# Kernel tuning notes

Measured on AMD Instinct MI355X. Metric: run time of the kernel, lower is better.

The kernel has to match this reference:

```python
import jax, jax.numpy as jnp
import numpy as np

N_NODES = 100000


def gcn_conv(x, W, b, src, dst, n_nodes):
    # PyG GCNConv: h = x @ W; add self-loops; sym-normalized scatter-add; + bias
    loop = jnp.arange(n_nodes, dtype=src.dtype)
    src2 = jnp.concatenate([src, loop])
    dst2 = jnp.concatenate([dst, loop])
    deg = jax.ops.segment_sum(jnp.ones(src2.shape, x.dtype), dst2, num_segments=n_nodes)
    dinv = jax.lax.rsqrt(deg)  # deg >= 1 thanks to self-loops
    norm = dinv[src2] * dinv[dst2]                 # [E+N]
    h = x @ W                                      # [N, out]
    msg = h[src2] * norm[:, None]                  # gather + scale, [E+N, out]
    out = jax.ops.segment_sum(msg, dst2, num_segments=n_nodes)  # scatter-add
    return out + b


def setup_inputs() -> dict:
    key = jax.random.key(0)
    k1, k2, k3, k4, k5 = jax.random.split(key, 5)
    nfeat, nhid = 128, 64
    n_edges = 1600000
    x = jax.random.normal(k1, (N_NODES, nfeat), dtype=jnp.float32)
    edge_index = jax.random.randint(k2, (2, n_edges), 0, N_NODES, dtype=jnp.int64)
    W1 = jax.random.normal(k3, (nfeat, nhid), dtype=jnp.float32) / np.sqrt(nfeat)
    b1 = jnp.zeros((nhid,), jnp.float32)
    W2 = jax.random.normal(k4, (nhid, nhid), dtype=jnp.float32) / np.sqrt(nhid)
    b2 = jnp.zeros((nhid,), jnp.float32)
    return {"x": x, "edge_index": edge_index, "W1": W1, "b1": b1, "W2": W2, "b2": b2}


def reference(x, edge_index, W1, b1, W2, b2):
    # eval mode: dropout is identity
    src, dst = edge_index[0], edge_index[1]
    h = jax.nn.relu(gcn_conv(x, W1, b1, src, dst, N_NODES))
    residual = h
    out = jax.nn.relu(gcn_conv(h, W2, b2, src, dst, N_NODES))
    return out + residual
```

## Files before the change

### kernel.cpp

```cpp
#include <hip/hip_runtime.h>

#define N_NODES 100000
#define NDUMMY 100000
#define NH 64
#define NB 500
#define NPB 200
#define BCAP 4096
#define PBCAP 6400
#define EPB 8192


__device__ __forceinline__ unsigned short f2bf(float f) {
    union { float f; unsigned int i; } c;
    c.f = f;
    unsigned int b = c.i;
    b += 0x7FFFu + ((b >> 16) & 1u);
    return (unsigned short)(b >> 16);
}

__device__ __forceinline__ unsigned pack2bf(float lo, float hi) {
    return (unsigned)f2bf(lo) | ((unsigned)f2bf(hi) << 16);
}

__device__ __forceinline__ float bfLO(unsigned u) {
    union { unsigned i; float f; } c; c.i = u << 16; return c.f;
}
__device__ __forceinline__ float bfHI(unsigned u) {
    union { unsigned i; float f; } c; c.i = u & 0xFFFF0000u; return c.f;
}


__global__ __launch_bounds__(512) void k_init(int* __restrict__ bcur, unsigned* __restrict__ dummy_row) {
    int t = threadIdx.x;
    if (t < NB) bcur[t] = 0;
    if (t < 32) dummy_row[t] = 0;
}


__global__ __launch_bounds__(1024) void k_sort(const int* __restrict__ src, const int* __restrict__ dst,
                                               int* __restrict__ bcur, unsigned* __restrict__ ebuf, int e) {
    __shared__ unsigned sorted[EPB];
    __shared__ unsigned short cellof[EPB];
    __shared__ int lh[512];
    __shared__ int lbase[512];
    __shared__ int lcur[512];
    __shared__ int gpos[512];
    __shared__ int wsum[8];
    const int t = threadIdx.x;
    const int e0 = blockIdx.x * EPB;
    int cnt = e - e0; if (cnt > EPB) cnt = EPB;

    if (t < 512) lh[t] = 0;
    __syncthreads();

    for (int i = t * 4; i < cnt; i += 4096) {
        int4 d4 = *(const int4*)&dst[e0 + i];
        atomicAdd(&lh[d4.x / NPB], 1);
        atomicAdd(&lh[d4.y / NPB], 1);
        atomicAdd(&lh[d4.z / NPB], 1);
        atomicAdd(&lh[d4.w / NPB], 1);
    }
    __syncthreads();

    const int lane = t & 63, wave = t >> 6;
    int v = 0, inc = 0;
    if (t < 512) {
        v = (t < NB) ? lh[t] : 0;
        inc = v;
#pragma unroll
        for (int d = 1; d < 64; d <<= 1) {
            int u = __shfl_up(inc, d, 64);
            if (lane >= d) inc += u;
        }
        if (lane == 63) wsum[wave] = inc;
    }
    __syncthreads();
    if (t < NB) {
        int woff = 0;
#pragma unroll
        for (int w = 0; w < 8; ++w)
            if (w < wave) woff += wsum[w];
        const int excl = woff + inc - v;
        lbase[t] = excl;
        lcur[t] = excl;
        gpos[t] = atomicAdd(&bcur[t], v);
    }
    __syncthreads();

    for (int i = t * 4; i < cnt; i += 4096) {
        int4 d4 = *(const int4*)&dst[e0 + i];
        int4 s4 = *(const int4*)&src[e0 + i];
        int b0 = d4.x / NPB, b1 = d4.y / NPB, b2 = d4.z / NPB, b3 = d4.w / NPB;
        int p0 = atomicAdd(&lcur[b0], 1);
        int p1 = atomicAdd(&lcur[b1], 1);
        int p2 = atomicAdd(&lcur[b2], 1);
        int p3 = atomicAdd(&lcur[b3], 1);
        sorted[p0] = ((unsigned)(d4.x - b0 * NPB) << 17) | (unsigned)s4.x; cellof[p0] = (unsigned short)b0;
        sorted[p1] = ((unsigned)(d4.y - b1 * NPB) << 17) | (unsigned)s4.y; cellof[p1] = (unsigned short)b1;
        sorted[p2] = ((unsigned)(d4.z - b2 * NPB) << 17) | (unsigned)s4.z; cellof[p2] = (unsigned short)b2;
        sorted[p3] = ((unsigned)(d4.w - b3 * NPB) << 17) | (unsigned)s4.w; cellof[p3] = (unsigned short)b3;
    }
    __syncthreads();

    for (int i = t * 4; i < cnt; i += 4096) {
        uint4 sv = *(const uint4*)&sorted[i];
        ushort4 cv = *(const ushort4*)&cellof[i];
        int c0 = cv.x, c1 = cv.y, c2 = cv.z, c3 = cv.w;
        int g0 = gpos[c0] + (i + 0 - lbase[c0]);
        int g1 = gpos[c1] + (i + 1 - lbase[c1]);
        int g2 = gpos[c2] + (i + 2 - lbase[c2]);
        int g3 = gpos[c3] + (i + 3 - lbase[c3]);
        if (g0 < BCAP) ebuf[(long long)c0 * BCAP + g0] = sv.x;
        if (g1 < BCAP) ebuf[(long long)c1 * BCAP + g1] = sv.y;
        if (g2 < BCAP) ebuf[(long long)c2 * BCAP + g2] = sv.z;
        if (g3 < BCAP) ebuf[(long long)c3 * BCAP + g3] = sv.w;
    }
}

__global__ __launch_bounds__(256) void k_build(const unsigned* __restrict__ ebuf, const int* __restrict__ bcur,
                                               int* __restrict__ rowptr, int* __restrict__ degp,
                                               float* __restrict__ dinv, int* __restrict__ csrc, int n) {
    __shared__ unsigned ls[BCAP];
    __shared__ int lh[256];
    __shared__ int lpv[256];
    __shared__ int lstart[256];
    __shared__ int lc[256];
    __shared__ int wsum[4];
    const int b = blockIdx.x;
    const int t = threadIdx.x;
    const int node0 = b * NPB;
    int count = bcur[b];
    if (count > BCAP) count = BCAP;
    const int rbase = b * PBCAP;

    lh[t] = 0;
    for (int i = t; i < count; i += 256) ls[i] = ebuf[(long long)b * BCAP + i];
    __syncthreads();
    for (int i = t; i < count; i += 256) atomicAdd(&lh[ls[i] >> 17], 1);
    __syncthreads();

    const int v = lh[t];
    lpv[t] = (v + 7) & ~7;
    __syncthreads();
    const int g = t & ~7;
    int pvg = lpv[g];
#pragma unroll
    for (int j = 1; j < 8; ++j) pvg = max(pvg, lpv[g + j]);

    const int lane = t & 63, wave = t >> 6;
    int inc = pvg;
#pragma unroll
    for (int d = 1; d < 64; d <<= 1) {
        int u = __shfl_up(inc, d, 64);
        if (lane >= d) inc += u;
    }
    if (lane == 63) wsum[wave] = inc;
    __syncthreads();
    int woff = 0;
#pragma unroll
    for (int w = 0; w < 4; ++w)
        if (w < wave) woff += wsum[w];
    const int start = rbase + woff + inc - pvg;

    lstart[t] = start;
    lc[t] = start;
    const int node = node0 + t;
    if (t < NPB && node < n) {
        rowptr[node] = start;
        degp[node] = pvg;
        dinv[node] = rsqrtf((float)(v + 1));
    }
    __syncthreads();

    for (int i = t; i < count; i += 256) {
        unsigned u = ls[i];
        int pos = atomicAdd(&lc[u >> 17], 1);
        csrc[pos] = (int)(u & 0x1FFFFu);
    }
    __syncthreads();

    const int pend = lstart[t] + pvg;
    for (int p = lc[t]; p < pend; ++p) csrc[p] = NDUMMY;
}


typedef __attribute__((ext_vector_type(8))) short bf16x8;
typedef __attribute__((ext_vector_type(4))) float f32x4;

template <int K>
__global__ __launch_bounds__(256) void k_gemm_mfma(const float* __restrict__ X, const float* __restrict__ W,
                                                   const float* __restrict__ dinv,
                                                   unsigned short* __restrict__ out, int n) {
    constexpr int KH = K / 2;
    constexpr int WP = (K == 128) ? 68 : 40;
    constexpr int NKS = K / 32;
    __shared__ unsigned wsb[64][WP];
    const int tid = threadIdx.x;
    const int lane = tid & 63;
    const int wv = tid >> 6;
    const int n0 = blockIdx.x * 64;
    const int col = lane & 15;
    const int q = lane >> 4;

    const int row = n0 + wv * 16 + col;
    const int rc = (row < n) ? row : (n - 1);
    const float* xp = X + (long long)rc * K + q * 8;
    float4 xa[NKS], xb[NKS];
#pragma unroll
    for (int ks = 0; ks < NKS; ++ks) {
        xa[ks] = *(const float4*)&xp[ks * 32];
        xb[ks] = *(const float4*)&xp[ks * 32 + 4];
    }

    for (int idx = tid; idx < 64 * KH; idx += 256) {
        int c = idx & 63, k2 = idx >> 6;
        wsb[c][k2] = pack2bf(W[(2 * k2) * NH + c], W[(2 * k2 + 1) * NH + c]);
    }

    union FragU { bf16x8 v; unsigned u[4]; };
    bf16x8 afrag[NKS];
#pragma unroll
    for (int ks = 0; ks < NKS; ++ks) {
        FragU f;
        f.u[0] = pack2bf(xa[ks].x, xa[ks].y);
        f.u[1] = pack2bf(xa[ks].z, xa[ks].w);
        f.u[2] = pack2bf(xb[ks].x, xb[ks].y);
        f.u[3] = pack2bf(xb[ks].z, xb[ks].w);
        afrag[ks] = f.v;
    }
    __syncthreads();

    f32x4 zero = {0.f, 0.f, 0.f, 0.f};
    f32x4 acc[4];
#pragma unroll
    for (int nt = 0; nt < 4; ++nt) acc[nt] = zero;

#pragma unroll
    for (int ks = 0; ks < NKS; ++ks) {
#pragma unroll
        for (int nt = 0; nt < 4; ++nt) {
            bf16x8 b = *(const bf16x8*)&wsb[nt * 16 + col][ks * 16 + q * 4];
            acc[nt] = __builtin_amdgcn_mfma_f32_16x16x32_bf16(afrag[ks], b, acc[nt], 0, 0, 0);
        }
    }

#pragma unroll
    for (int r = 0; r < 4; ++r) {
        int node = n0 + wv * 16 + q * 4 + r;
        if (node < n) {
            float dv = dinv[node];
#pragma unroll
            for (int nt = 0; nt < 4; ++nt)
                out[(long long)node * NH + nt * 16 + col] = f2bf(acc[nt][r] * dv);
        }
    }
}


__global__ __launch_bounds__(256) void k_agg(const unsigned* __restrict__ hs32, const float* __restrict__ dinv,
                                             const int* __restrict__ rowptr, const int* __restrict__ degp,
                                             const int* __restrict__ csrc,
                                             const float* __restrict__ bias, const float* __restrict__ resid,
                                             float* __restrict__ out, int n) {
    const int gt = blockIdx.x * 256 + threadIdx.x;
    const int wave = gt >> 6;
    const int lane = threadIdx.x & 63;
    const int sub = lane >> 3;
    const int li = lane & 7;
    const int node = wave * 8 + sub;
    if (node >= n) return;

    const uint4* hsv = (const uint4*)hs32;
    uint4 su = hsv[node * 8 + li];
    float a0 = bfLO(su.x), a1 = bfHI(su.x), a2 = bfLO(su.y), a3 = bfHI(su.y);
    float a4 = bfLO(su.z), a5 = bfHI(su.z), a6 = bfLO(su.w), a7 = bfHI(su.w);
    float b0 = 0.f, b1 = 0.f, b2 = 0.f, b3 = 0.f, b4 = 0.f, b5 = 0.f, b6 = 0.f, b7 = 0.f;

    const int rp = rowptr[node];
    const int dg = degp[node];
    int4 c0, c1;
    if (dg > 0) {
        c0 = *(const int4*)&csrc[rp];
        c1 = *(const int4*)&csrc[rp + 4];
    }
    for (int e = 0; e < dg; e += 8) {
        const int4 m0 = c0, m1 = c1;
        if (e + 8 < dg) {
            c0 = *(const int4*)&csrc[rp + e + 8];
            c1 = *(const int4*)&csrc[rp + e + 12];
        }
        uint4 u0 = hsv[m0.x * 8 + li];
        uint4 u1 = hsv[m0.y * 8 + li];
        uint4 u2 = hsv[m0.z * 8 + li];
        uint4 u3 = hsv[m0.w * 8 + li];
        uint4 u4 = hsv[m1.x * 8 + li];
        uint4 u5 = hsv[m1.y * 8 + li];
        uint4 u6 = hsv[m1.z * 8 + li];
        uint4 u7 = hsv[m1.w * 8 + li];
        a0 += bfLO(u0.x); a1 += bfHI(u0.x); a2 += bfLO(u0.y); a3 += bfHI(u0.y);
        a4 += bfLO(u0.z); a5 += bfHI(u0.z); a6 += bfLO(u0.w); a7 += bfHI(u0.w);
        b0 += bfLO(u1.x); b1 += bfHI(u1.x); b2 += bfLO(u1.y); b3 += bfHI(u1.y);
        b4 += bfLO(u1.z); b5 += bfHI(u1.z); b6 += bfLO(u1.w); b7 += bfHI(u1.w);
        a0 += bfLO(u2.x); a1 += bfHI(u2.x); a2 += bfLO(u2.y); a3 += bfHI(u2.y);
        a4 += bfLO(u2.z); a5 += bfHI(u2.z); a6 += bfLO(u2.w); a7 += bfHI(u2.w);
        b0 += bfLO(u3.x); b1 += bfHI(u3.x); b2 += bfLO(u3.y); b3 += bfHI(u3.y);
        b4 += bfLO(u3.z); b5 += bfHI(u3.z); b6 += bfLO(u3.w); b7 += bfHI(u3.w);
        a0 += bfLO(u4.x); a1 += bfHI(u4.x); a2 += bfLO(u4.y); a3 += bfHI(u4.y);
        a4 += bfLO(u4.z); a5 += bfHI(u4.z); a6 += bfLO(u4.w); a7 += bfHI(u4.w);
        b0 += bfLO(u5.x); b1 += bfHI(u5.x); b2 += bfLO(u5.y); b3 += bfHI(u5.y);
        b4 += bfLO(u5.z); b5 += bfHI(u5.z); b6 += bfLO(u5.w); b7 += bfHI(u5.w);
        a0 += bfLO(u6.x); a1 += bfHI(u6.x); a2 += bfLO(u6.y); a3 += bfHI(u6.y);
        a4 += bfLO(u6.z); a5 += bfHI(u6.z); a6 += bfLO(u6.w); a7 += bfHI(u6.w);
        b0 += bfLO(u7.x); b1 += bfHI(u7.x); b2 += bfLO(u7.y); b3 += bfHI(u7.y);
        b4 += bfLO(u7.z); b5 += bfHI(u7.z); b6 += bfLO(u7.w); b7 += bfHI(u7.w);
    }
    const float dv = dinv[node];
    const float4 ba = *(const float4*)&bias[8 * li];
    const float4 bb = *(const float4*)&bias[8 * li + 4];
    float v0 = fmaxf(dv * (a0 + b0) + ba.x, 0.f);
    float v1 = fmaxf(dv * (a1 + b1) + ba.y, 0.f);
    float v2 = fmaxf(dv * (a2 + b2) + ba.z, 0.f);
    float v3 = fmaxf(dv * (a3 + b3) + ba.w, 0.f);
    float v4 = fmaxf(dv * (a4 + b4) + bb.x, 0.f);
    float v5 = fmaxf(dv * (a5 + b5) + bb.y, 0.f);
    float v6 = fmaxf(dv * (a6 + b6) + bb.z, 0.f);
    float v7 = fmaxf(dv * (a7 + b7) + bb.w, 0.f);
    const long long ob = (long long)node * NH + 8 * li;
    if (resid) {
        float4 r0 = *(const float4*)&resid[ob];
        float4 r1 = *(const float4*)&resid[ob + 4];
        v0 += r0.x; v1 += r0.y; v2 += r0.z; v3 += r0.w;
        v4 += r1.x; v5 += r1.y; v6 += r1.z; v7 += r1.w;
    }
    *(float4*)&out[ob] = make_float4(v0, v1, v2, v3);
    *(float4*)&out[ob + 4] = make_float4(v4, v5, v6, v7);
}


extern "C" void kernel_launch(void* const* d_in, const int* in_sizes, int n_in,
                              void* d_out, int out_size, void* d_ws, size_t ws_size,
                              hipStream_t stream) {
    const float* x  = (const float*)d_in[0];
    const int*   ei = (const int*)d_in[1];
    const float* W1 = (const float*)d_in[2];
    const float* b1 = (const float*)d_in[3];
    const float* W2 = (const float*)d_in[4];
    const float* b2 = (const float*)d_in[5];
    float* out = (float*)d_out;

    const int N = N_NODES;
    const int E = in_sizes[1] / 2;
    const int* src = ei;
    const int* dst = ei + E;

    const int NP = 100352;
    int*   bcur   = (int*)d_ws;
    int*   rowptr = bcur + 512;
    int*   degp   = rowptr + NP;
    float* dinv   = (float*)(degp + NP);
    int*   csrc   = (int*)(dinv + NP);
    unsigned* ebuf = (unsigned*)(csrc + NB * PBCAP);
    unsigned* hs32 = ebuf;
    unsigned short* hsb = (unsigned short*)hs32;
    float* h1     = (float*)(hs32 + (long long)(NDUMMY + 1) * 32);

    const int nb_sort = (E + EPB - 1) / EPB;

    k_init<<<1, 512, 0, stream>>>(bcur, hs32 + (long long)NDUMMY * 32);
    k_sort<<<nb_sort, 1024, 0, stream>>>(src, dst, bcur, ebuf, E);
    k_build<<<NB, 256, 0, stream>>>(ebuf, bcur, rowptr, degp, dinv, csrc, N);

    k_gemm_mfma<128><<<(N + 63) / 64, 256, 0, stream>>>(x, W1, dinv, hsb, N);
    k_agg<<<(N + 31) / 32, 256, 0, stream>>>(hs32, dinv, rowptr, degp, csrc, b1, nullptr, h1, N);

    k_gemm_mfma<64><<<(N + 63) / 64, 256, 0, stream>>>(h1, W2, dinv, hsb, N);
    k_agg<<<(N + 31) / 32, 256, 0, stream>>>(hs32, dinv, rowptr, degp, csrc, b2, h1, out, N);
}
```

Before: 131.3 us.

## Split bf16 feature table into two 32-column halves for cache-friendlier aggregation

The GEMM now writes the bf16 hidden features as two separate planes, each holding 32 columns per node, and the aggregation kernel launches twice as many blocks, each block handling one half. Each gathered plane is half the size of the full table, so it is more likely to stay resident in L2/MALL while the random neighbour gathers run. In exchange, every neighbour index is read twice, per-lane loads shrink from 16 to 8 bytes, and the workspace is reordered so the sort buffer aliases h1.

```diff
diff --git a/kernel.cpp b/kernel.cpp
--- a/kernel.cpp
+++ b/kernel.cpp
@@ -2,6 +2,7 @@
 
 #define N_NODES 100000
 #define NDUMMY 100000
+#define NROWS 100001
 #define NH 64
 #define NB 500
 #define NPB 200
@@ -30,10 +31,14 @@
 }
 
 
-__global__ __launch_bounds__(512) void k_init(int* __restrict__ bcur, unsigned* __restrict__ dummy_row) {
+__global__ __launch_bounds__(512) void k_init(int* __restrict__ bcur, unsigned* __restrict__ hs32) {
     int t = threadIdx.x;
     if (t < NB) bcur[t] = 0;
-    if (t < 32) dummy_row[t] = 0;
+    if (t >= 512 - 32) {
+        int j = t - (512 - 32);
+        int h = j >> 4, w = j & 15;
+        hs32[(long long)h * NROWS * 16 + (long long)NDUMMY * 16 + w] = 0;
+    }
 }
 
 
@@ -250,8 +255,11 @@
         if (node < n) {
             float dv = dinv[node];
 #pragma unroll
-            for (int nt = 0; nt < 4; ++nt)
-                out[(long long)node * NH + nt * 16 + col] = f2bf(acc[nt][r] * dv);
+            for (int nt = 0; nt < 4; ++nt) {
+                int c = nt * 16 + col;
+                long long addr = (long long)(c >> 5) * NROWS * 32 + (long long)node * 32 + (c & 31);
+                out[addr] = f2bf(acc[nt][r] * dv);
+            }
         }
     }
 }
@@ -262,19 +270,19 @@
                                              const int* __restrict__ csrc,
                                              const float* __restrict__ bias, const float* __restrict__ resid,
                                              float* __restrict__ out, int n) {
-    const int gt = blockIdx.x * 256 + threadIdx.x;
-    const int wave = gt >> 6;
+    const int h = blockIdx.x & 1;
+    const int nb = blockIdx.x >> 1;
+    const int wave_in_blk = threadIdx.x >> 6;
     const int lane = threadIdx.x & 63;
     const int sub = lane >> 3;
     const int li = lane & 7;
-    const int node = wave * 8 + sub;
+    const int node = nb * 32 + wave_in_blk * 8 + sub;
     if (node >= n) return;
 
-    const uint4* hsv = (const uint4*)hs32;
-    uint4 su = hsv[node * 8 + li];
+    const uint2* hsv = (const uint2*)(hs32 + (long long)h * NROWS * 16);
+    uint2 su = hsv[node * 8 + li];
     float a0 = bfLO(su.x), a1 = bfHI(su.x), a2 = bfLO(su.y), a3 = bfHI(su.y);
-    float a4 = bfLO(su.z), a5 = bfHI(su.z), a6 = bfLO(su.w), a7 = bfHI(su.w);
-    float b0 = 0.f, b1 = 0.f, b2 = 0.f, b3 = 0.f, b4 = 0.f, b5 = 0.f, b6 = 0.f, b7 = 0.f;
+    float b0 = 0.f, b1 = 0.f, b2 = 0.f, b3 = 0.f;
 
     const int rp = rowptr[node];
     const int dg = degp[node];
@@ -289,51 +297,36 @@
             c0 = *(const int4*)&csrc[rp + e + 8];
             c1 = *(const int4*)&csrc[rp + e + 12];
         }
-        uint4 u0 = hsv[m0.x * 8 + li];
-        uint4 u1 = hsv[m0.y * 8 + li];
-        uint4 u2 = hsv[m0.z * 8 + li];
-        uint4 u3 = hsv[m0.w * 8 + li];
-        uint4 u4 = hsv[m1.x * 8 + li];
-        uint4 u5 = hsv[m1.y * 8 + li];
-        uint4 u6 = hsv[m1.z * 8 + li];
-        uint4 u7 = hsv[m1.w * 8 + li];
+        uint2 u0 = hsv[m0.x * 8 + li];
+        uint2 u1 = hsv[m0.y * 8 + li];
+        uint2 u2 = hsv[m0.z * 8 + li];
+        uint2 u3 = hsv[m0.w * 8 + li];
+        uint2 u4 = hsv[m1.x * 8 + li];
+        uint2 u5 = hsv[m1.y * 8 + li];
+        uint2 u6 = hsv[m1.z * 8 + li];
+        uint2 u7 = hsv[m1.w * 8 + li];
         a0 += bfLO(u0.x); a1 += bfHI(u0.x); a2 += bfLO(u0.y); a3 += bfHI(u0.y);
-        a4 += bfLO(u0.z); a5 += bfHI(u0.z); a6 += bfLO(u0.w); a7 += bfHI(u0.w);
         b0 += bfLO(u1.x); b1 += bfHI(u1.x); b2 += bfLO(u1.y); b3 += bfHI(u1.y);
-        b4 += bfLO(u1.z); b5 += bfHI(u1.z); b6 += bfLO(u1.w); b7 += bfHI(u1.w);
         a0 += bfLO(u2.x); a1 += bfHI(u2.x); a2 += bfLO(u2.y); a3 += bfHI(u2.y);
-        a4 += bfLO(u2.z); a5 += bfHI(u2.z); a6 += bfLO(u2.w); a7 += bfHI(u2.w);
         b0 += bfLO(u3.x); b1 += bfHI(u3.x); b2 += bfLO(u3.y); b3 += bfHI(u3.y);
-        b4 += bfLO(u3.z); b5 += bfHI(u3.z); b6 += bfLO(u3.w); b7 += bfHI(u3.w);
         a0 += bfLO(u4.x); a1 += bfHI(u4.x); a2 += bfLO(u4.y); a3 += bfHI(u4.y);
-        a4 += bfLO(u4.z); a5 += bfHI(u4.z); a6 += bfLO(u4.w); a7 += bfHI(u4.w);
         b0 += bfLO(u5.x); b1 += bfHI(u5.x); b2 += bfLO(u5.y); b3 += bfHI(u5.y);
-        b4 += bfLO(u5.z); b5 += bfHI(u5.z); b6 += bfLO(u5.w); b7 += bfHI(u5.w);
         a0 += bfLO(u6.x); a1 += bfHI(u6.x); a2 += bfLO(u6.y); a3 += bfHI(u6.y);
-        a4 += bfLO(u6.z); a5 += bfHI(u6.z); a6 += bfLO(u6.w); a7 += bfHI(u6.w);
         b0 += bfLO(u7.x); b1 += bfHI(u7.x); b2 += bfLO(u7.y); b3 += bfHI(u7.y);
-        b4 += bfLO(u7.z); b5 += bfHI(u7.z); b6 += bfLO(u7.w); b7 += bfHI(u7.w);
     }
     const float dv = dinv[node];
-    const float4 ba = *(const float4*)&bias[8 * li];
-    const float4 bb = *(const float4*)&bias[8 * li + 4];
-    float v0 = fmaxf(dv * (a0 + b0) + ba.x, 0.f);
-    float v1 = fmaxf(dv * (a1 + b1) + ba.y, 0.f);
-    float v2 = fmaxf(dv * (a2 + b2) + ba.z, 0.f);
-    float v3 = fmaxf(dv * (a3 + b3) + ba.w, 0.f);
-    float v4 = fmaxf(dv * (a4 + b4) + bb.x, 0.f);
-    float v5 = fmaxf(dv * (a5 + b5) + bb.y, 0.f);
-    float v6 = fmaxf(dv * (a6 + b6) + bb.z, 0.f);
-    float v7 = fmaxf(dv * (a7 + b7) + bb.w, 0.f);
-    const long long ob = (long long)node * NH + 8 * li;
+    const int fb = h * 32 + li * 4;
+    const float4 bb = *(const float4*)&bias[fb];
+    float v0 = fmaxf(dv * (a0 + b0) + bb.x, 0.f);
+    float v1 = fmaxf(dv * (a1 + b1) + bb.y, 0.f);
+    float v2 = fmaxf(dv * (a2 + b2) + bb.z, 0.f);
+    float v3 = fmaxf(dv * (a3 + b3) + bb.w, 0.f);
+    const long long ob = (long long)node * NH + fb;
     if (resid) {
-        float4 r0 = *(const float4*)&resid[ob];
-        float4 r1 = *(const float4*)&resid[ob + 4];
-        v0 += r0.x; v1 += r0.y; v2 += r0.z; v3 += r0.w;
-        v4 += r1.x; v5 += r1.y; v6 += r1.z; v7 += r1.w;
+        float4 rr = *(const float4*)&resid[ob];
+        v0 += rr.x; v1 += rr.y; v2 += rr.z; v3 += rr.w;
     }
     *(float4*)&out[ob] = make_float4(v0, v1, v2, v3);
-    *(float4*)&out[ob + 4] = make_float4(v4, v5, v6, v7);
 }
 
 
@@ -359,20 +352,20 @@
     int*   degp   = rowptr + NP;
     float* dinv   = (float*)(degp + NP);
     int*   csrc   = (int*)(dinv + NP);
-    unsigned* ebuf = (unsigned*)(csrc + NB * PBCAP);
-    unsigned* hs32 = ebuf;
+    unsigned* hs32 = (unsigned*)(csrc + NB * PBCAP);
+    float* h1     = (float*)(hs32 + (long long)2 * NROWS * 16);
+    unsigned* ebuf = (unsigned*)h1;
     unsigned short* hsb = (unsigned short*)hs32;
-    float* h1     = (float*)(hs32 + (long long)(NDUMMY + 1) * 32);
 
     const int nb_sort = (E + EPB - 1) / EPB;
 
-    k_init<<<1, 512, 0, stream>>>(bcur, hs32 + (long long)NDUMMY * 32);
+    k_init<<<1, 512, 0, stream>>>(bcur, hs32);
     k_sort<<<nb_sort, 1024, 0, stream>>>(src, dst, bcur, ebuf, E);
     k_build<<<NB, 256, 0, stream>>>(ebuf, bcur, rowptr, degp, dinv, csrc, N);
 
     k_gemm_mfma<128><<<(N + 63) / 64, 256, 0, stream>>>(x, W1, dinv, hsb, N);
-    k_agg<<<(N + 31) / 32, 256, 0, stream>>>(hs32, dinv, rowptr, degp, csrc, b1, nullptr, h1, N);
+    k_agg<<<((N + 31) / 32) * 2, 256, 0, stream>>>(hs32, dinv, rowptr, degp, csrc, b1, nullptr, h1, N);
 
     k_gemm_mfma<64><<<(N + 63) / 64, 256, 0, stream>>>(h1, W2, dinv, hsb, N);
-    k_agg<<<(N + 31) / 32, 256, 0, stream>>>(hs32, dinv, rowptr, degp, csrc, b2, h1, out, N);
-}
+    k_agg<<<((N + 31) / 32) * 2, 256, 0, stream>>>(hs32, dinv, rowptr, degp, csrc, b2, h1, out, N);
+}
```

Measured after the change: 147.7 us. +12.5%, slower.
